# Performance work log

Hardware: AMD Instinct MI355X
Metric: run time of the kernel (lower is better)

## Reference

```python
import jax, jax.numpy as jnp
import numpy as np

H_FEAT, W_FEAT, C_FEAT = 96, 96, 64
UP = 4
HQ, WQ = H_FEAT * UP, W_FEAT * UP
HID, DEPTH = 64, 2
MOD_DIM = HID * 2 * DEPTH          # scale + shift per hidden layer -> 256
HYP_IN = C_FEAT * 9 + 2            # unfolded feat + rel_cell -> 578
HYP_HID = 256


def make_coord(h, w):
    # pixel-center coords in [-1,1], order (y, x) matching (h, w)
    y = ((jnp.arange(h, dtype=jnp.float32) + 0.5) / h) * 2.0 - 1.0
    x = ((jnp.arange(w, dtype=jnp.float32) + 0.5) / w) * 2.0 - 1.0
    yy, xx = jnp.meshgrid(y, x, indexing='ij')
    return jnp.stack([yy, xx], axis=-1)  # (h, w, 2)


def _unfold3(feat):
    # F.unfold(feat, 3, padding=1).view(B, C*9, h, w): channel-major patch order
    B, C, h, w = feat.shape
    p = jnp.pad(feat, ((0, 0), (0, 0), (1, 1), (1, 1)))
    patches = jnp.stack([p[:, :, dy:dy + h, dx:dx + w]
                         for dy in range(3) for dx in range(3)], axis=2)
    return patches.reshape(B, C * 9, h, w)


def _gather_nearest(img, coord):
    # grid_sample(img, coord.flip(-1), mode='nearest', align_corners=False)
    # img: (B, C, H, W); coord: (B, Q, 2) in (y, x) order, range [-1, 1]
    B, C, H, W = img.shape
    iy = jnp.clip(jnp.round((coord[..., 0] + 1.0) * H / 2.0 - 0.5), 0, H - 1).astype(jnp.int32)
    ix = jnp.clip(jnp.round((coord[..., 1] + 1.0) * W / 2.0 - 0.5), 0, W - 1).astype(jnp.int32)
    idx = (iy * W + ix)[:, None, :]                      # (B, 1, Q)
    out = jnp.take_along_axis(img.reshape(B, C, H * W), idx, axis=2)
    return out.transpose(0, 2, 1)                        # (B, Q, C)


def setup_inputs() -> dict:
    key = jax.random.key(0)
    ks = jax.random.split(key, 6)
    s = 0.02
    feat = jax.random.normal(ks[0], (1, C_FEAT, H_FEAT, W_FEAT), jnp.float32)
    coord = make_coord(HQ, WQ).reshape(1, HQ * WQ, 2)
    cell = jnp.broadcast_to(jnp.array([2.0 / HQ, 2.0 / WQ], jnp.float32),
                            (1, HQ * WQ, 2)).astype(jnp.float32)
    return {
        'feat': feat, 'coord': coord, 'cell': cell,
        'Wh1': jax.random.normal(ks[1], (HYP_IN, HYP_HID), jnp.float32) * s,
        'bh1': jnp.zeros((HYP_HID,), jnp.float32),
        'Wh2': jax.random.normal(ks[2], (HYP_HID, MOD_DIM), jnp.float32) * s,
        'bh2': jnp.zeros((MOD_DIM,), jnp.float32),
        'W0': jax.random.normal(ks[3], (C_FEAT + 4, HID), jnp.float32) * s,
        'b0': jnp.zeros((HID,), jnp.float32),
        'W1': jax.random.normal(ks[4], (HID, HID), jnp.float32) * s,
        'b1': jnp.zeros((HID,), jnp.float32),
        'W2': jax.random.normal(ks[5], (HID, 3), jnp.float32) * s,
        'b2': jnp.zeros((3,), jnp.float32),
    }


def reference(feat, coord, cell, Wh1, bh1, Wh2, bh2, W0, b0, W1, b1, W2, b2):
    B, C, h, w = feat.shape
    hw_scale = jnp.array([h, w], jnp.float32)

    # --- gen_feats: 3x3 unfold for the hypernet input ---
    rich = _unfold3(feat)                                   # (B, 9C, h, w)

    # --- gen_modulations: per-latent-pixel hypernet MLP ---
    hyp_in = rich.transpose(0, 2, 3, 1).reshape(B, h * w, C * 9)
    rel_cell_lr = cell[:, :h * w, :] * hw_scale             # cell_decode
    hyp_in = jnp.concatenate([hyp_in, rel_cell_lr], axis=-1)
    mod = jax.nn.relu(hyp_in @ Wh1 + bh1) @ Wh2 + bh2       # (B, h*w, MOD_DIM)
    mod = mod.reshape(B, h, w, MOD_DIM).transpose(0, 3, 1, 2)

    feat_coord = jnp.broadcast_to(
        make_coord(h, w).transpose(2, 0, 1)[None], (B, 2, h, w))

    # --- query_rgb: local-ensemble gather -> modulated MLP -> area blend ---
    rx, ry = 1.0 / h, 1.0 / w                               # 2/h/2, 2/w/2
    eps = 1e-6
    rel_cell_q = cell * hw_scale                            # (B, Q, 2)
    preds, areas = [], []
    for vx in (-1.0, 1.0):
        for vy in (-1.0, 1.0):
            c_ = coord + jnp.array([vx * rx + eps, vy * ry + eps], jnp.float32)
            c_ = jnp.clip(c_, -1.0 + 1e-6, 1.0 - 1e-6)
            q_feat = _gather_nearest(feat, c_)              # (B, Q, C)
            q_coord = _gather_nearest(feat_coord, c_)       # (B, Q, 2)
            q_mod = _gather_nearest(mod, c_)                # (B, Q, MOD_DIM)
            rel = (coord - q_coord) * hw_scale              # (B, Q, 2)
            x = jnp.concatenate([q_feat, rel, rel_cell_q], axis=-1)
            # imnet: hidden layers modulated by (scale, shift) from hypernet
            x = x @ W0 + b0
            x = jax.nn.relu(x * q_mod[..., 0:HID] + q_mod[..., 2 * HID:3 * HID])
            x = x @ W1 + b1
            x = jax.nn.relu(x * q_mod[..., HID:2 * HID] + q_mod[..., 3 * HID:4 * HID])
            preds.append(x @ W2 + b2)                       # (B, Q, 3)
            areas.append(jnp.abs(rel[..., 0] * rel[..., 1]) + 1e-9)

    # diagonal-swap of ensemble areas (LIIF local ensemble)
    areas[0], areas[3] = areas[3], areas[0]
    areas[1], areas[2] = areas[2], areas[1]
    tot = areas[0] + areas[1] + areas[2] + areas[3]
    out = sum(p * (a / tot)[..., None] for p, a in zip(preds, areas))
    return out  # (B, Q, 3)
```

## Files before the change

### kernel.cpp

```cpp
#include <hip/hip_runtime.h>


#define HW 96
#define NPIX (96*96)
#define CFEAT 64
#define INV192 (1.0f/192.0f)

typedef __attribute__((ext_vector_type(8))) short short8;
typedef __attribute__((ext_vector_type(4))) float f32x4;

__device__ __forceinline__ unsigned pack_bf2(float a, float b) {
    unsigned ua = __builtin_bit_cast(unsigned, a);
    unsigned ub = __builtin_bit_cast(unsigned, b);
    return (ua >> 16) | (ub & 0xffff0000u);
}
__device__ __forceinline__ float bf_hi(float a) {
    return __builtin_bit_cast(float, __builtin_bit_cast(unsigned, a) & 0xffff0000u);
}
__device__ __forceinline__ void split8(const float (&v)[8], short8& hi, short8& lo) {
    union { short8 s; unsigned u[4]; } H, L;
    #pragma unroll
    for (int p = 0; p < 4; ++p) {
        float a = v[2*p], b = v[2*p+1];
        H.u[p] = pack_bf2(a, b);
        L.u[p] = pack_bf2(a - bf_hi(a), b - bf_hi(b));
    }
    hi = H.s; lo = L.s;
}
__device__ __forceinline__ unsigned rne16(float x) {
    unsigned u = __builtin_bit_cast(unsigned, x);
    return (u + 0x7fffu + ((u >> 16) & 1u)) >> 16;
}
__device__ __forceinline__ unsigned pack_bf2_rne(float a, float b) {
    return rne16(a) | (rne16(b) << 16);
}
__device__ __forceinline__ short top16(float a) {
    return (short)(__builtin_bit_cast(unsigned, a) >> 16);
}

__device__ __forceinline__ float dpp_red16(float v) {
    int x;
    x = __builtin_amdgcn_update_dpp(0, __builtin_bit_cast(int, v), 0xB1, 0xF, 0xF, true);
    v += __builtin_bit_cast(float, x);
    x = __builtin_amdgcn_update_dpp(0, __builtin_bit_cast(int, v), 0x4E, 0xF, 0xF, true);
    v += __builtin_bit_cast(float, x);
    x = __builtin_amdgcn_update_dpp(0, __builtin_bit_cast(int, v), 0x141, 0xF, 0xF, true);
    v += __builtin_bit_cast(float, x);
    x = __builtin_amdgcn_update_dpp(0, __builtin_bit_cast(int, v), 0x140, 0xF, 0xF, true);
    v += __builtin_bit_cast(float, x);
    return v;
}

#define AXCALC(CV, SGN, II, RR)                                        \
{                                                                      \
    float e = CV + (SGN)*(1.0f/96.0f) + 1e-6f;                         \
    e = fminf(fmaxf(e, -1.0f + 1e-6f), 1.0f - 1e-6f);                  \
    II = (int)rintf((e + 1.0f) * 48.0f - 0.5f);                        \
    II = min(max(II, 0), 95);                                          \
    RR = (CV - fmaf((float)II, 0.0208333333f, -0.9895833333f)) * 96.0f;\
}

__global__ __launch_bounds__(256) void swizzle_kernel(
    const float* __restrict__ Wh1, const float* __restrict__ Wh2,
    const float* __restrict__ W0, short* __restrict__ wsw)
{
    const int gid = blockIdx.x*256 + threadIdx.x;
    if (gid >= 424*64) return;
    const int f    = gid >> 6;
    const int lane = gid & 63;
    const int c    = lane & 15;
    const int kg   = lane >> 4;
    const float* W; int kt, nt, N;
    if (f < 288)      { W = Wh1; kt = f >> 4;        nt = f & 15;        N = 256; }
    else if (f < 416) { W = Wh2; kt = (f-288) >> 4;  nt = (f-288) & 15;  N = 256; }
    else              { W = W0;  kt = (f-416) >> 2;  nt = (f-416) & 3;   N = 64;  }
    union { short8 s; unsigned u[4]; } H;
    #pragma unroll
    for (int p = 0; p < 4; ++p) {
        float a = W[(kt*32 + kg*8 + 2*p    )*N + nt*16 + c];
        float b = W[(kt*32 + kg*8 + 2*p + 1)*N + nt*16 + c];
        H.u[p] = pack_bf2_rne(a, b);
    }
    *(short8*)(wsw + (size_t)f*512 + lane*8) = H.s;
}

__global__ __launch_bounds__(512) void hyper_mfma(
    const float* __restrict__ feat,
    const float* __restrict__ cell,
    const float* __restrict__ Wh1,
    const float* __restrict__ bh1,
    const float* __restrict__ bh2,
    const float* __restrict__ b0,
    const short* __restrict__ wsw,
    float* __restrict__ mod_ws,
    float* __restrict__ f0_ws)
{
    __shared__ short AHI[72*128];
    __shared__ short ALO[72*128];
    __shared__ short HHI[32*128];
    __shared__ short HLO[32*128];

    const int tid = threadIdx.x;
    const int blk = blockIdx.x;
    const int y   = blk / 6;
    const int x0  = (blk % 6) * 16;
    const int qbase = y*HW + x0;

    for (int idx = tid; idx < 9216; idx += 512) {
        const int px = idx & 15;
        const int k  = idx >> 4;
        const int ch = k / 9;
        const int j  = k - 9*ch;
        const int dy = j / 3;
        const int dx = j - 3*dy;
        const int gy = y + dy - 1;
        const int gx = x0 + px + dx - 1;
        float v = 0.0f;
        if (gy >= 0 && gy < HW && gx >= 0 && gx < HW)
            v = feat[ch*NPIX + gy*HW + gx];
        const int dst = (k >> 3)*128 + px*8 + (k & 7);
        AHI[dst] = top16(v);
        ALO[dst] = top16(v - bf_hi(v));
    }
    __syncthreads();

    const int lane = tid & 63;
    const int wid  = tid >> 6;
    const int c    = lane & 15;
    const int kg   = lane >> 4;

    const short* wh1f = wsw;
    const short* wh2f = wsw + (size_t)288*512;
    const short* w0f  = wsw + (size_t)416*512;

    if (wid < 4) {
        f32x4 acc0;
        const float bb = b0[wid*16 + c];
        acc0[0] = bb; acc0[1] = bb; acc0[2] = bb; acc0[3] = bb;
        #pragma unroll
        for (int kt = 0; kt < 2; ++kt) {
            float v[8];
            #pragma unroll
            for (int j = 0; j < 8; ++j)
                v[j] = feat[(kt*32 + kg*8 + j)*NPIX + y*HW + x0 + c];
            short8 Ahi, Alo;
            split8(v, Ahi, Alo);
            const short8 B = *(const short8*)(w0f + (size_t)(kt*4 + wid)*512 + lane*8);
            acc0 = __builtin_amdgcn_mfma_f32_16x16x32_bf16(Ahi, B, acc0, 0, 0, 0);
            acc0 = __builtin_amdgcn_mfma_f32_16x16x32_bf16(Alo, B, acc0, 0, 0, 0);
        }
        #pragma unroll
        for (int i = 0; i < 4; ++i)
            f0_ws[(size_t)(qbase + kg*4 + i)*64 + wid*16 + c] = acc0[i];
    }

    f32x4 acc[2];
    #pragma unroll
    for (int nt = 0; nt < 2; ++nt) {
        const float bb = bh1[wid*32 + nt*16 + c];
        acc[nt][0] = bb; acc[nt][1] = bb; acc[nt][2] = bb; acc[nt][3] = bb;
    }
    #pragma unroll
    for (int kt = 0; kt < 18; ++kt) {
        const int aoff = (kt*4 + kg)*128 + c*8;
        const short8 Ahi = *(const short8*)&AHI[aoff];
        const short8 Alo = *(const short8*)&ALO[aoff];
        #pragma unroll
        for (int nt = 0; nt < 2; ++nt) {
            const short8 B = *(const short8*)(wh1f + (size_t)(kt*16 + wid*2 + nt)*512 + lane*8);
            acc[nt] = __builtin_amdgcn_mfma_f32_16x16x32_bf16(Ahi, B, acc[nt], 0, 0, 0);
            acc[nt] = __builtin_amdgcn_mfma_f32_16x16x32_bf16(Alo, B, acc[nt], 0, 0, 0);
        }
    }
    {
        float rc0v[4], rc1v[4];
        #pragma unroll
        for (int i = 0; i < 4; ++i) {
            const int q = qbase + kg*4 + i;
            const float2 ce = ((const float2*)cell)[q];
            rc0v[i] = ce.x * 96.0f;
            rc1v[i] = ce.y * 96.0f;
        }
        #pragma unroll
        for (int nt = 0; nt < 2; ++nt) {
            const int n = wid*32 + nt*16 + c;
            const float w5 = Wh1[576*256 + n];
            const float w6 = Wh1[577*256 + n];
            #pragma unroll
            for (int i = 0; i < 4; ++i) {
                float hv = acc[nt][i] + rc0v[i]*w5 + rc1v[i]*w6;
                hv = fmaxf(hv, 0.0f);
                const int dst = (n >> 3)*128 + (kg*4 + i)*8 + (n & 7);
                HHI[dst] = top16(hv);
                HLO[dst] = top16(hv - bf_hi(hv));
            }
        }
    }
    __syncthreads();

    f32x4 acc2[2];
    #pragma unroll
    for (int nt = 0; nt < 2; ++nt) {
        const float bb = bh2[wid*32 + nt*16 + c];
        acc2[nt][0] = bb; acc2[nt][1] = bb; acc2[nt][2] = bb; acc2[nt][3] = bb;
    }
    #pragma unroll
    for (int kt = 0; kt < 8; ++kt) {
        const int aoff = (kt*4 + kg)*128 + c*8;
        const short8 Ahi = *(const short8*)&HHI[aoff];
        const short8 Alo = *(const short8*)&HLO[aoff];
        #pragma unroll
        for (int nt = 0; nt < 2; ++nt) {
            const short8 B = *(const short8*)(wh2f + (size_t)(kt*16 + wid*2 + nt)*512 + lane*8);
            acc2[nt] = __builtin_amdgcn_mfma_f32_16x16x32_bf16(Ahi, B, acc2[nt], 0, 0, 0);
            acc2[nt] = __builtin_amdgcn_mfma_f32_16x16x32_bf16(Alo, B, acc2[nt], 0, 0, 0);
        }
    }
    #pragma unroll
    for (int nt = 0; nt < 2; ++nt) {
        #pragma unroll
        for (int i = 0; i < 4; ++i)
            mod_ws[(size_t)(qbase + kg*4 + i)*256 + wid*32 + nt*16 + c] = acc2[nt][i];
    }
}

#define ROWQ 324

__global__ __launch_bounds__(256) void query_kernel_v7(
    const float* __restrict__ cell,
    const float* __restrict__ W0,
    const float* __restrict__ W1,
    const float* __restrict__ b1,
    const float* __restrict__ W2,
    const float* __restrict__ b2,
    const float* __restrict__ mod_ws,
    const float* __restrict__ f0_ws,
    float* __restrict__ out)
{
    __shared__ float smem[24*ROWQ];

    const int tid = threadIdx.x;
    const int bX  = blockIdx.x % 48;
    const int bY  = blockIdx.x / 48;
    const int X0  = bX * 8;
    const int Y0  = bY * 16;
    const int lx0 = bX*2 - 1;
    const int ly0 = bY*4 - 1;

    const float rc0 = cell[0] * 96.0f;
    const float rc1 = cell[1] * 96.0f;

    const float4* w64p = (const float4*)(W0 + 64*64);
    const float4* w65p = (const float4*)(W0 + 65*64);
    const float4* w66p = (const float4*)(W0 + 66*64);
    const float4* w67p = (const float4*)(W0 + 67*64);

    for (int idx = tid; idx < 1536; idx += 256) {
        const int r  = idx >> 6;
        const int o  = idx & 63;
        const int ry = r >> 2;
        const int rx = r & 3;
        const int gy = min(max(ly0 + ry, 0), 95);
        const int gx = min(max(lx0 + rx, 0), 95);
        const int src = gy*96 + gx;
        const float4* modv = (const float4*)(mod_ws + (size_t)src*256);
        if (o < 16) {
            const float4 f0 = ((const float4*)(f0_ws + (size_t)src*64))[o];
            const float4 s1 = modv[o];
            const float4 t1 = modv[32 + o];
            const float4 a  = w66p[o];
            const float4 b  = w67p[o];
            float4 v;
            v.x = fmaf(s1.x, fmaf(rc1, b.x, fmaf(rc0, a.x, f0.x)), t1.x);
            v.y = fmaf(s1.y, fmaf(rc1, b.y, fmaf(rc0, a.y, f0.y)), t1.y);
            v.z = fmaf(s1.z, fmaf(rc1, b.z, fmaf(rc0, a.z, f0.z)), t1.z);
            v.w = fmaf(s1.w, fmaf(rc1, b.w, fmaf(rc0, a.w, f0.w)), t1.w);
            *(float4*)(smem + r*ROWQ + o*4) = v;
        } else if (o < 32) {
            const int oo = o - 16;
            const float4 s1 = modv[oo];
            const float4 w  = w64p[oo];
            float4 v = {s1.x*w.x, s1.y*w.y, s1.z*w.z, s1.w*w.w};
            *(float4*)(smem + r*ROWQ + 64 + oo*4) = v;
        } else if (o < 48) {
            const int oo = o - 32;
            const float4 s1 = modv[oo];
            const float4 w  = w65p[oo];
            float4 v = {s1.x*w.x, s1.y*w.y, s1.z*w.z, s1.w*w.w};
            *(float4*)(smem + r*ROWQ + 128 + oo*4) = v;
        } else {
            const int oo = o - 48;
            const float4 s2 = modv[16 + oo];
            const float4 h2 = modv[48 + oo];
            #pragma unroll
            for (int j = 0; j < 4; ++j) {
                const int col = oo*4 + j;
                const int cc  = col & 15;
                const int nt  = col >> 4;
                const float sv = (j==0)?s2.x:(j==1)?s2.y:(j==2)?s2.z:s2.w;
                const float hv = (j==0)?h2.x:(j==1)?h2.y:(j==2)?h2.z:h2.w;
                smem[r*ROWQ + 192 + cc*4 + nt] = sv;
                smem[r*ROWQ + 256 + cc*4 + nt] = hv;
            }
        }
    }

    const int lane = tid & 63;
    const int wid  = tid >> 6;
    const int c    = lane & 15;
    const int kg   = lane >> 4;

    short8 Bh[4][2];
    #pragma unroll
    for (int nt = 0; nt < 4; ++nt) {
        #pragma unroll
        for (int kt = 0; kt < 2; ++kt) {
            union { short8 s; unsigned u[4]; } H;
            #pragma unroll
            for (int p = 0; p < 4; ++p) {
                float a = W1[(kt*32 + kg*8 + 2*p    )*64 + nt*16 + c];
                float b = W1[(kt*32 + kg*8 + 2*p + 1)*64 + nt*16 + c];
                H.u[p] = pack_bf2_rne(a, b);
            }
            Bh[nt][kt] = H.s;
        }
    }
    float b1c[4];
    float w2r[4][3];
    #pragma unroll
    for (int nt = 0; nt < 4; ++nt) {
        b1c[nt] = b1[nt*16 + c];
        w2r[nt][0] = W2[(nt*16 + c)*3 + 0];
        w2r[nt][1] = W2[(nt*16 + c)*3 + 1];
        w2r[nt][2] = W2[(nt*16 + c)*3 + 2];
    }
    const float b2v0 = b2[0], b2v1 = b2[1], b2v2 = b2[2];

    __syncthreads();

    const int Xw   = X0 + (wid & 1)*4;
    const int Yw   = Y0 + (wid >> 1)*8;
    const int qxA  = c >> 2;
    const int tapA = c & 3;
    const float vxA = (tapA < 2) ? -1.0f : 1.0f;
    const float vyA = (tapA & 1) ? 1.0f : -1.0f;

    const float cxA = ((float)(Xw + qxA) + 0.5f) * INV192 - 1.0f;
    const float cxE = ((float)(Xw + kg)  + 0.5f) * INV192 - 1.0f;
    int ixA; float r1A;
    AXCALC(cxA, vyA, ixA, r1A)
    const int ixAc = ixA - lx0;
    int ixm, ixp; float r1m, r1p;
    AXCALC(cxE, -1.0f, ixm, r1m)
    AXCALC(cxE,  1.0f, ixp, r1p)

    #pragma unroll 2
    for (int m = 0; m < 8; ++m) {
        const int qy = Yw + m;
        const float cy = ((float)qy + 0.5f) * INV192 - 1.0f;

        short8 Ahi[2], Alo[2];
        {
            int iyA; float r0A;
            AXCALC(cy, vxA, iyA, r0A)
            const float* rowp = smem + ((iyA - ly0)*4 + ixAc) * ROWQ;
            #pragma unroll
            for (int kt = 0; kt < 2; ++kt) {
                const int kb = kt*32 + kg*8;
                const float4 ga  = *(const float4*)(rowp + kb);
                const float4 gb  = *(const float4*)(rowp + kb + 4);
                const float4 u0a = *(const float4*)(rowp + 64  + kb);
                const float4 u0b = *(const float4*)(rowp + 64  + kb + 4);
                const float4 u1a = *(const float4*)(rowp + 128 + kb);
                const float4 u1b = *(const float4*)(rowp + 128 + kb + 4);
                float g[8]  = {ga.x,ga.y,ga.z,ga.w,gb.x,gb.y,gb.z,gb.w};
                float u0[8] = {u0a.x,u0a.y,u0a.z,u0a.w,u0b.x,u0b.y,u0b.z,u0b.w};
                float u1[8] = {u1a.x,u1a.y,u1a.z,u1a.w,u1b.x,u1b.y,u1b.z,u1b.w};
                float hv[8];
                #pragma unroll
                for (int j = 0; j < 8; ++j) {
                    float pre = fmaf(r0A, u0[j], g[j]);
                    pre = fmaf(r1A, u1[j], pre);
                    hv[j] = fmaxf(pre, 0.f);
                }
                split8(hv, Ahi[kt], Alo[kt]);
            }
        }

        int iym, iyp; float r0m, r0p;
        AXCALC(cy, -1.0f, iym, r0m)
        AXCALC(cy,  1.0f, iyp, r0p)
        const int rym = (iym - ly0)*4 - lx0;
        const int ryp = (iyp - ly0)*4 - lx0;
        const int lr0 = rym + ixm, lr1 = rym + ixp;
        const int lr2 = ryp + ixm, lr3 = ryp + ixp;
        float4 sc2v[4], sh2v[4];
        #pragma unroll
        for (int i = 0; i < 4; ++i) {
            const int lri = (i == 0) ? lr0 : (i == 1) ? lr1 : (i == 2) ? lr2 : lr3;
            sc2v[i] = *(const float4*)(smem + lri*ROWQ + 192 + c*4);
            sh2v[i] = *(const float4*)(smem + lri*ROWQ + 256 + c*4);
        }
        const float a0 = fabsf(r0m*r1m) + 1e-9f;
        const float a1 = fabsf(r0m*r1p) + 1e-9f;
        const float a2 = fabsf(r0p*r1m) + 1e-9f;
        const float a3 = fabsf(r0p*r1p) + 1e-9f;
        const float invt = 1.0f / (a0 + a1 + a2 + a3);
        const float w0_ = a3 * invt, w1_ = a2 * invt, w2_ = a1 * invt, w3_ = a0 * invt;

        f32x4 acc[4];
        #pragma unroll
        for (int nt = 0; nt < 4; ++nt) {
            f32x4 z = {b1c[nt], b1c[nt], b1c[nt], b1c[nt]};
            acc[nt] = z;
        }
        #pragma unroll
        for (int nt = 0; nt < 4; ++nt) {
            #pragma unroll
            for (int kt = 0; kt < 2; ++kt) {
                acc[nt] = __builtin_amdgcn_mfma_f32_16x16x32_bf16(Ahi[kt], Bh[nt][kt], acc[nt], 0, 0, 0);
                acc[nt] = __builtin_amdgcn_mfma_f32_16x16x32_bf16(Alo[kt], Bh[nt][kt], acc[nt], 0, 0, 0);
            }
        }

        float p0 = 0.f, p1 = 0.f, p2 = 0.f;
        #pragma unroll
        for (int i = 0; i < 4; ++i) {
            const float wi = (i == 0) ? w0_ : (i == 1) ? w1_ : (i == 2) ? w2_ : w3_;
            float s0 = 0.f, s1 = 0.f, s2 = 0.f;
            #pragma unroll
            for (int nt = 0; nt < 4; ++nt) {
                const float sc2 = (nt==0)?sc2v[i].x:(nt==1)?sc2v[i].y:(nt==2)?sc2v[i].z:sc2v[i].w;
                const float sh2 = (nt==0)?sh2v[i].x:(nt==1)?sh2v[i].y:(nt==2)?sh2v[i].z:sh2v[i].w;
                const float v = fmaxf(fmaf(acc[nt][i], sc2, sh2), 0.f);
                s0 = fmaf(v, w2r[nt][0], s0);
                s1 = fmaf(v, w2r[nt][1], s1);
                s2 = fmaf(v, w2r[nt][2], s2);
            }
            p0 = fmaf(s0, wi, p0);
            p1 = fmaf(s1, wi, p1);
            p2 = fmaf(s2, wi, p2);
        }
        p0 = dpp_red16(p0);
        p1 = dpp_red16(p1);
        p2 = dpp_red16(p2);
        if (c < 3) {
            const int qE = qy*384 + Xw + kg;
            const float ov = (c == 0) ? p0 + b2v0 : (c == 1) ? p1 + b2v1 : p2 + b2v2;
            out[(size_t)qE*3 + c] = ov;
        }
    }
}

extern "C" void kernel_launch(void* const* d_in, const int* in_sizes, int n_in,
                              void* d_out, int out_size, void* d_ws, size_t ws_size,
                              hipStream_t stream) {
    const float* feat  = (const float*)d_in[0];
    const float* cell  = (const float*)d_in[2];
    const float* Wh1   = (const float*)d_in[3];
    const float* bh1   = (const float*)d_in[4];
    const float* Wh2   = (const float*)d_in[5];
    const float* bh2   = (const float*)d_in[6];
    const float* W0    = (const float*)d_in[7];
    const float* b0    = (const float*)d_in[8];
    const float* W1    = (const float*)d_in[9];
    const float* b1    = (const float*)d_in[10];
    const float* W2    = (const float*)d_in[11];
    const float* b2    = (const float*)d_in[12];
    float* out = (float*)d_out;

    float* mod_ws = (float*)d_ws;
    float* f0_ws  = (float*)d_ws + 9216*256;
    short* wsw    = (short*)((char*)d_ws + 11796480);

    swizzle_kernel<<<dim3(106), dim3(256), 0, stream>>>(Wh1, Wh2, W0, wsw);
    hyper_mfma<<<dim3(576), dim3(512), 0, stream>>>(
        feat, cell, Wh1, bh1, bh2, b0, wsw, mod_ws, f0_ws);
    query_kernel_v7<<<dim3(1152), dim3(256), 0, stream>>>(
        cell, W0, W1, b1, W2, b2, mod_ws, f0_ws, out);
}
```

Baseline: 79.33 us.

## Use single bf16 MFMA pass and preswizzled W1 in query kernel

The query kernel's first hidden layer drops the hi/lo bf16 split of the activations and runs one MFMA pass per tile, halving the MFMA work there. W1 is now converted and swizzled once by the swizzle kernel instead of being packed from fp32 in every block. The ensemble-weight and shift/scale loads are moved ahead of the activation build, and the unroll factor goes from 2 to 4. The cost is lower precision in that layer, because activations are rounded to bf16 without a compensation term, plus a somewhat larger swizzle launch.

```diff
diff --git a/kernel.cpp b/kernel.cpp
--- a/kernel.cpp
+++ b/kernel.cpp
@@ -62,10 +62,11 @@
 
 __global__ __launch_bounds__(256) void swizzle_kernel(
     const float* __restrict__ Wh1, const float* __restrict__ Wh2,
-    const float* __restrict__ W0, short* __restrict__ wsw)
+    const float* __restrict__ W0, const float* __restrict__ W1,
+    short* __restrict__ wsw)
 {
     const int gid = blockIdx.x*256 + threadIdx.x;
-    if (gid >= 424*64) return;
+    if (gid >= 432*64) return;
     const int f    = gid >> 6;
     const int lane = gid & 63;
     const int c    = lane & 15;
@@ -73,7 +74,8 @@
     const float* W; int kt, nt, N;
     if (f < 288)      { W = Wh1; kt = f >> 4;        nt = f & 15;        N = 256; }
     else if (f < 416) { W = Wh2; kt = (f-288) >> 4;  nt = (f-288) & 15;  N = 256; }
-    else              { W = W0;  kt = (f-416) >> 2;  nt = (f-416) & 3;   N = 64;  }
+    else if (f < 424) { W = W0;  kt = (f-416) >> 2;  nt = (f-416) & 3;   N = 64;  }
+    else              { W = W1;  kt = (f-424) >> 2;  nt = (f-424) & 3;   N = 64;  }
     union { short8 s; unsigned u[4]; } H;
     #pragma unroll
     for (int p = 0; p < 4; ++p) {
@@ -226,10 +228,10 @@
 
 #define ROWQ 324
 
-__global__ __launch_bounds__(256) void query_kernel_v7(
+__global__ __launch_bounds__(256) void query_kernel_v8(
     const float* __restrict__ cell,
     const float* __restrict__ W0,
-    const float* __restrict__ W1,
+    const short* __restrict__ wsw,
     const float* __restrict__ b1,
     const float* __restrict__ W2,
     const float* __restrict__ b2,
@@ -310,21 +312,14 @@
     const int c    = lane & 15;
     const int kg   = lane >> 4;
 
+    const short* w1f = wsw + (size_t)424*512;
     short8 Bh[4][2];
     #pragma unroll
-    for (int nt = 0; nt < 4; ++nt) {
-        #pragma unroll
-        for (int kt = 0; kt < 2; ++kt) {
-            union { short8 s; unsigned u[4]; } H;
-            #pragma unroll
-            for (int p = 0; p < 4; ++p) {
-                float a = W1[(kt*32 + kg*8 + 2*p    )*64 + nt*16 + c];
-                float b = W1[(kt*32 + kg*8 + 2*p + 1)*64 + nt*16 + c];
-                H.u[p] = pack_bf2_rne(a, b);
-            }
-            Bh[nt][kt] = H.s;
-        }
-    }
+    for (int kt = 0; kt < 2; ++kt)
+        #pragma unroll
+        for (int nt = 0; nt < 4; ++nt)
+            Bh[nt][kt] = *(const short8*)(w1f + (size_t)(kt*4 + nt)*512 + lane*8);
+
     float b1c[4];
     float w2r[4][3];
     #pragma unroll
@@ -354,12 +349,33 @@
     AXCALC(cxE, -1.0f, ixm, r1m)
     AXCALC(cxE,  1.0f, ixp, r1p)
 
-    #pragma unroll 2
+    #pragma unroll 4
     for (int m = 0; m < 8; ++m) {
         const int qy = Yw + m;
         const float cy = ((float)qy + 0.5f) * INV192 - 1.0f;
 
-        short8 Ahi[2], Alo[2];
+        int iym, iyp; float r0m, r0p;
+        AXCALC(cy, -1.0f, iym, r0m)
+        AXCALC(cy,  1.0f, iyp, r0p)
+        const int rym = (iym - ly0)*4 - lx0;
+        const int ryp = (iyp - ly0)*4 - lx0;
+        const int lr0 = rym + ixm, lr1 = rym + ixp;
+        const int lr2 = ryp + ixm, lr3 = ryp + ixp;
+        float4 sc2v[4], sh2v[4];
+        #pragma unroll
+        for (int i = 0; i < 4; ++i) {
+            const int lri = (i == 0) ? lr0 : (i == 1) ? lr1 : (i == 2) ? lr2 : lr3;
+            sc2v[i] = *(const float4*)(smem + lri*ROWQ + 192 + c*4);
+            sh2v[i] = *(const float4*)(smem + lri*ROWQ + 256 + c*4);
+        }
+        const float a0 = fabsf(r0m*r1m) + 1e-9f;
+        const float a1 = fabsf(r0m*r1p) + 1e-9f;
+        const float a2 = fabsf(r0p*r1m) + 1e-9f;
+        const float a3 = fabsf(r0p*r1p) + 1e-9f;
+        const float invt = 1.0f / (a0 + a1 + a2 + a3);
+        const float w0_ = a3 * invt, w1_ = a2 * invt, w2_ = a1 * invt, w3_ = a0 * invt;
+
+        short8 A[2];
         {
             int iyA; float r0A;
             AXCALC(cy, vxA, iyA, r0A)
@@ -383,30 +399,13 @@
                     pre = fmaf(r1A, u1[j], pre);
                     hv[j] = fmaxf(pre, 0.f);
                 }
-                split8(hv, Ahi[kt], Alo[kt]);
+                union { short8 s; unsigned u[4]; } P;
+                #pragma unroll
+                for (int p = 0; p < 4; ++p)
+                    P.u[p] = pack_bf2_rne(hv[2*p], hv[2*p+1]);
+                A[kt] = P.s;
             }
         }
-
-        int iym, iyp; float r0m, r0p;
-        AXCALC(cy, -1.0f, iym, r0m)
-        AXCALC(cy,  1.0f, iyp, r0p)
-        const int rym = (iym - ly0)*4 - lx0;
-        const int ryp = (iyp - ly0)*4 - lx0;
-        const int lr0 = rym + ixm, lr1 = rym + ixp;
-        const int lr2 = ryp + ixm, lr3 = ryp + ixp;
-        float4 sc2v[4], sh2v[4];
-        #pragma unroll
-        for (int i = 0; i < 4; ++i) {
-            const int lri = (i == 0) ? lr0 : (i == 1) ? lr1 : (i == 2) ? lr2 : lr3;
-            sc2v[i] = *(const float4*)(smem + lri*ROWQ + 192 + c*4);
-            sh2v[i] = *(const float4*)(smem + lri*ROWQ + 256 + c*4);
-        }
-        const float a0 = fabsf(r0m*r1m) + 1e-9f;
-        const float a1 = fabsf(r0m*r1p) + 1e-9f;
-        const float a2 = fabsf(r0p*r1m) + 1e-9f;
-        const float a3 = fabsf(r0p*r1p) + 1e-9f;
-        const float invt = 1.0f / (a0 + a1 + a2 + a3);
-        const float w0_ = a3 * invt, w1_ = a2 * invt, w2_ = a1 * invt, w3_ = a0 * invt;
 
         f32x4 acc[4];
         #pragma unroll
@@ -417,10 +416,8 @@
         #pragma unroll
         for (int nt = 0; nt < 4; ++nt) {
             #pragma unroll
-            for (int kt = 0; kt < 2; ++kt) {
-                acc[nt] = __builtin_amdgcn_mfma_f32_16x16x32_bf16(Ahi[kt], Bh[nt][kt], acc[nt], 0, 0, 0);
-                acc[nt] = __builtin_amdgcn_mfma_f32_16x16x32_bf16(Alo[kt], Bh[nt][kt], acc[nt], 0, 0, 0);
-            }
+            for (int kt = 0; kt < 2; ++kt)
+                acc[nt] = __builtin_amdgcn_mfma_f32_16x16x32_bf16(A[kt], Bh[nt][kt], acc[nt], 0, 0, 0);
         }
 
         float p0 = 0.f, p1 = 0.f, p2 = 0.f;
@@ -473,9 +470,9 @@
     float* f0_ws  = (float*)d_ws + 9216*256;
     short* wsw    = (short*)((char*)d_ws + 11796480);
 
-    swizzle_kernel<<<dim3(106), dim3(256), 0, stream>>>(Wh1, Wh2, W0, wsw);
+    swizzle_kernel<<<dim3(108), dim3(256), 0, stream>>>(Wh1, Wh2, W0, W1, wsw);
     hyper_mfma<<<dim3(576), dim3(512), 0, stream>>>(
         feat, cell, Wh1, bh1, bh2, b0, wsw, mod_ws, f0_ws);
-    query_kernel_v7<<<dim3(1152), dim3(256), 0, stream>>>(
-        cell, W0, W1, b1, W2, b2, mod_ws, f0_ws, out);
-}
+    query_kernel_v8<<<dim3(1152), dim3(256), 0, stream>>>(
+        cell, W0, wsw, b1, W2, b2, mod_ws, f0_ws, out);
+}
```

New measurement: 76.73 us. -3.3%, faster.
